# Kernel optimization log

Measured on AMD Instinct MI355X. Metric: run time of the kernel, lower is better.

## Reference

```python
import jax, jax.numpy as jnp
import numpy as np

S, B, R, H, TOP, CHL = 512, 32, 8, 128, 3, 19
I = CHL + 1  # GRU input size after null-channel concat


def setup_inputs() -> dict:
    key = jax.random.key(0)
    ks = jax.random.split(key, 12)
    f = lambda k, shp, sc=0.05: jax.random.normal(k, shp, dtype=jnp.float32) * sc
    return {
        "x": f(ks[0], (B, CHL, S), 1.0),
        "Wih": f(ks[1], (R, 3 * H, I)),      # per-rim GRU input weights (torch order r,z,n)
        "Whh": f(ks[2], (R, 3 * H, H)),      # per-rim GRU hidden weights
        "Qir_w": f(ks[3], (H, H)),
        "Qir_b": f(ks[4], (H,)),
        "Kir_w": f(ks[5], (H, S)),
        "Vir_w": f(ks[6], (H, S)),
        "Qrr_w": f(ks[7], (H, H)),
        "Krr_w": f(ks[8], (H, H)),
        "Vrr_w": f(ks[9], (H, H)),
    }


def reference(x, Wih, Whh, Qir_w, Qir_b, Kir_w, Vir_w, Qrr_w, Krr_w, Vrr_w):
    Bn = x.shape[0]
    # prepend null channel, reshape to (S, B, I)
    xc = jnp.concatenate([jnp.zeros((Bn, 1, x.shape[2]), x.dtype), x], axis=1)
    xs = jnp.transpose(xc, (2, 0, 1))  # (S, B, I)

    # ---- per-rim GRU (no bias), torch gate order (r, z, n) ----
    x_proj = jnp.einsum('sbi,rgi->srbg', xs, Wih)  # (S, R, B, 3H)

    def step(hprev, xp):
        hp = jnp.einsum('rbh,rgh->rbg', hprev, Whh)
        xr, xz, xn = jnp.split(xp, 3, axis=-1)
        hr, hz, hn = jnp.split(hp, 3, axis=-1)
        r = jax.nn.sigmoid(xr + hr)
        z = jax.nn.sigmoid(xz + hz)
        n = jnp.tanh(xn + r * hn)
        hnew = (1.0 - z) * n + z * hprev
        return hnew, hnew

    h0 = jnp.zeros((R, Bn, H), x.dtype)
    _, hs = jax.lax.scan(step, h0, x_proj)      # (S, R, B, H)
    h = jnp.transpose(hs, (1, 0, 2, 3))          # (R, S, B, H)

    # ---- stage one: input attention + rim competition ----
    x_bis = jnp.transpose(xs, (1, 2, 0))         # (B, I, S)
    q = jnp.einsum('rsbh,oh->rsbo', h, Qir_w) + Qir_b
    k = jnp.einsum('bis,os->bio', x_bis, Kir_w)
    v = jnp.einsum('bis,os->bio', x_bis, Vir_w)
    qk = jnp.einsum('rsbh,bih->sbri', q, k) / (H ** 0.5)
    soft = jax.nn.softmax(qk, axis=3)            # (S, B, R, I)
    idx = jax.lax.top_k(-soft[..., 0], TOP)[1]   # (S, B, TOP)
    mask = jnp.sum(jax.nn.one_hot(idx, R, dtype=jnp.float32), axis=-2)[..., None]  # (S,B,R,1)
    mask = jax.lax.stop_gradient(mask)
    qkv = jnp.einsum('sbri,bih->sbrh', soft, v)  # (S, B, R, H)

    # NoGrad: forward identity, backward grad*mask
    h1 = qkv * mask + jax.lax.stop_gradient(qkv * (1.0 - mask))

    # ---- stage two: rim-rim attention, masked ----
    q2 = jnp.einsum('sbrh,oh->sbro', h1, Qrr_w)
    k2 = jnp.einsum('sbrh,oh->sbro', h1, Krr_w)
    v2 = jnp.einsum('sbrh,oh->sbro', h1, Vrr_w)
    qk2 = jnp.einsum('sbrh,sbch->sbrc', q2, k2)  # (S, B, R, R), no scaling (as in source)
    soft2 = jax.nn.softmax(qk2, axis=3) * mask
    out = h1 + jnp.einsum('sbrc,sbch->sbrh', soft2, v2)
    return out * mask
```

## Files before the change

kernel.cpp:

```cpp
#include <hip/hip_runtime.h>
#include <math.h>


typedef float v2f __attribute__((ext_vector_type(2)));

#define PKF(acc, w, h) \
    asm("v_pk_fma_f32 %0, %1, %2, %0" : "+v"(acc) : "v"(w), "v"(h))

__global__ void kT(const float* __restrict__ Kir, const float* __restrict__ Vir,
                   const float* __restrict__ Vrr,
                   float* __restrict__ KirT, float* __restrict__ VirT,
                   float* __restrict__ VrrT) {
    int idx = blockIdx.x * 256 + threadIdx.x;
    if (idx < 65536) {
        int s = idx >> 7, o = idx & 127;
        KirT[idx] = Kir[o * 512 + s];
    } else if (idx < 131072) {
        int j = idx - 65536;
        int s = j >> 7, o = j & 127;
        VirT[j] = Vir[o * 512 + s];
    } else if (idx < 147456) {
        int j = idx - 131072;
        int g = j >> 7, h = j & 127;
        VrrT[j] = Vrr[h * 128 + g];
    }
}

__global__ __launch_bounds__(128) void kKV(const float* __restrict__ x,
        const float* __restrict__ KirT, const float* __restrict__ VirT,
        float* __restrict__ kbuf, float* __restrict__ vbuf) {
    const int b = blockIdx.x / 20, i = blockIdx.x % 20;
    const int o = threadIdx.x;
    if (i == 0) {
        kbuf[(b * 20) * 128 + o] = 0.0f;
        vbuf[(b * 20) * 128 + o] = 0.0f;
        return;
    }
    __shared__ float xL[512];
    for (int idx = threadIdx.x; idx < 512; idx += 128)
        xL[idx] = x[(b * 19 + (i - 1)) * 512 + idx];
    __syncthreads();
    float ak = 0.0f, av = 0.0f;
#pragma unroll 4
    for (int s = 0; s < 512; ++s) {
        float xv = xL[s];
        ak += xv * KirT[s * 128 + o];
        av += xv * VirT[s * 128 + o];
    }
    kbuf[(b * 20 + i) * 128 + o] = ak;
    vbuf[(b * 20 + i) * 128 + o] = av;
}

__global__ __launch_bounds__(128) void kKQ(const float* __restrict__ kbuf,
        const float* __restrict__ Qir, const float* __restrict__ Qib,
        float* __restrict__ KQ, float* __restrict__ cb) {
    const int b = blockIdx.x / 20, i = blockIdx.x % 20;
    const int h = threadIdx.x;
    __shared__ float kL[128];
    kL[h] = kbuf[(b * 20 + i) * 128 + h];
    __syncthreads();
    float acc = 0.0f;
#pragma unroll 4
    for (int o = 0; o < 128; ++o) acc += kL[o] * Qir[o * 128 + h];
    KQ[(b * 20 + i) * 128 + h] = acc;
    if (h == 0) {
        float c = 0.0f;
        for (int o = 0; o < 128; ++o) c += kL[o] * Qib[o];
        cb[b * 20 + i] = c;
    }
}

__global__ __launch_bounds__(256) void kM(const float* __restrict__ Qrr,
        const float* __restrict__ Krr, float* __restrict__ M) {
    const int h = blockIdx.x * 2 + (threadIdx.x >> 7);
    const int g = threadIdx.x & 127;
    float acc = 0.0f;
#pragma unroll 4
    for (int o = 0; o < 128; ++o) acc += Qrr[o * 128 + h] * Krr[o * 128 + g];
    M[h * 128 + g] = acc;
}

template<int CTRL>
__device__ __forceinline__ float dppadd(float v) {
    int r = __builtin_amdgcn_update_dpp(0, __float_as_int(v), CTRL, 0xF, 0xF, true);
    return v + __int_as_float(r);
}
template<int CTRL>
__device__ __forceinline__ float dppbcast(float v) {
    int r = __builtin_amdgcn_update_dpp(0, __float_as_int(v), CTRL, 0xF, 0xF, true);
    return __int_as_float(r);
}

__global__ __launch_bounds__(512, 2) void kGRU(const float* __restrict__ x,
        const float* __restrict__ Wih, const float* __restrict__ Whh,
        float* __restrict__ hs) {
    const int r = blockIdx.x >> 5;
    const int b = blockIdx.x & 31;
    const int t = threadIdx.x;
    const int j = t >> 2;
    const int kq = t & 3;

    __shared__ __align__(16) float xT[512 * 20];
    __shared__ __align__(16) float hsBuf[64 * 144];

    for (int idx = t; idx < 19 * 512; idx += 512) {
        int c = idx >> 9, s = idx & 511;
        xT[s * 20 + c] = x[(b * 19 + c) * 512 + s];
    }
    if (t < 144) hsBuf[63 * 144 + t] = 0.0f;

    v2f w0[16], w1[16], w2[16];
    {
        const float* Wb = Whh + (r * 384) * 128 + kq * 32;
        const v2f* s0p = (const v2f*)(Wb + (j) * 128);
        const v2f* s1p = (const v2f*)(Wb + (j + 128) * 128);
        const v2f* s2p = (const v2f*)(Wb + (j + 256) * 128);
#pragma unroll
        for (int u = 0; u < 16; ++u) {
            w0[u] = s0p[u];
            w1[u] = s1p[u];
            w2[u] = s2p[u];
        }
    }
    v2f wiv[9];
    float wlast;
    if (kq < 3) {
        const float* W = Wih + (r * 384 + (j + 128 * kq)) * 20;
#pragma unroll
        for (int c = 0; c < 9; ++c) wiv[c] = (v2f){W[2*c + 1], W[2*c + 2]};
        wlast = W[19];
    } else {
#pragma unroll
        for (int c = 0; c < 9; ++c) wiv[c] = (v2f){0.0f, 0.0f};
        wlast = 0.0f;
    }
    __syncthreads();

    const int jmap = j + ((j >> 5) << 2);
    const int cellBase = (b * 8 + r) * 128;
    float hprev = 0.0f;

    for (int s = 0; s < 512; ++s) {
        const int rowR = (s + 63) & 63;
        const v2f* hp2 = (const v2f*)(hsBuf + rowR * 144 + kq * 36);
        v2f hv[16];
#pragma unroll
        for (int u = 0; u < 16; ++u) hv[u] = hp2[u];

        float xp;
        {
            const v2f* xp2 = (const v2f*)(xT + s * 20);
            float x18 = xT[s * 20 + 18];
            v2f xacc = {0.0f, 0.0f};
            PKF(xacc, wiv[0], xp2[0]);
            PKF(xacc, wiv[1], xp2[1]);
            PKF(xacc, wiv[2], xp2[2]);
            PKF(xacc, wiv[3], xp2[3]);
            PKF(xacc, wiv[4], xp2[4]);
            PKF(xacc, wiv[5], xp2[5]);
            PKF(xacc, wiv[6], xp2[6]);
            PKF(xacc, wiv[7], xp2[7]);
            PKF(xacc, wiv[8], xp2[8]);
            xp = xacc[0] + xacc[1] + wlast * x18;
        }

        v2f a0 = {0.0f, 0.0f}, a1 = {0.0f, 0.0f}, a2 = {0.0f, 0.0f};
#pragma unroll
        for (int u = 0; u < 16; ++u) {
            v2f hh = hv[u];
            PKF(a0, w0[u], hh);
            PKF(a1, w1[u], hh);
            PKF(a2, w2[u], hh);
        }
        float p0 = a0[0] + a0[1];
        float p1 = a1[0] + a1[1];
        float p2 = a2[0] + a2[1];

        p0 = dppadd<0xB1>(p0); p1 = dppadd<0xB1>(p1); p2 = dppadd<0xB1>(p2);
        p0 = dppadd<0x4E>(p0); p1 = dppadd<0x4E>(p1); p2 = dppadd<0x4E>(p2);
        float xr = dppbcast<0x00>(xp);
        float xz = dppbcast<0x55>(xp);
        float xn = dppbcast<0xAA>(xp);

        float rg = __builtin_amdgcn_rcpf(1.0f + __expf(-(p0 + xr)));
        float zg = __builtin_amdgcn_rcpf(1.0f + __expf(-(p1 + xz)));
        float a  = xn + rg * p2;
        float ng = 1.0f - 2.0f * __builtin_amdgcn_rcpf(__expf(2.0f * a) + 1.0f);
        float hnew = ng + zg * (hprev - ng);
        hprev = hnew;
        if (kq == 0) hsBuf[(s & 63) * 144 + jmap] = hnew;
        __syncthreads();

        if ((s & 63) == 63) {
            const int sBase = s - 63;
            const int c4 = (t & 31) * 4;
            const int cm = c4 + ((c4 >> 5) << 2);
#pragma unroll
            for (int w = 0; w < 4; ++w) {
                int rr = (t >> 5) + w * 16;
                float4 v = *(const float4*)(hsBuf + rr * 144 + cm);
                *(float4*)(hs + (size_t)(sBase + rr) * 32768 + cellBase + c4) = v;
            }
            __syncthreads();
        }
    }
}

__global__ __launch_bounds__(256) void kS1(const float* __restrict__ hs,
        const float* __restrict__ KQ, const float* __restrict__ cb,
        const float* __restrict__ vbuf,
        float* __restrict__ h1, int* __restrict__ widx, float* __restrict__ out) {
    const int b = blockIdx.x & 31;
    const int s0 = (blockIdx.x >> 5) * 16;
    const int t = threadIdx.x;
    __shared__ float KQL[20 * 132];
    __shared__ float vL[20 * 128];
    __shared__ float cbL[20];
    __shared__ float hLt[8 * 132];
    __shared__ float qkL[8 * 20];
    __shared__ float sfL[8 * 20];
    __shared__ float s0L[8];
    __shared__ int wselL[3];

    for (int idx = t; idx < 2560; idx += 256) {
        int i = idx >> 7, h = idx & 127;
        KQL[i * 132 + h] = KQ[(b * 20 + i) * 128 + h];
        vL[i * 128 + h] = vbuf[(b * 20 + i) * 128 + h];
    }
    if (t < 20) cbL[t] = cb[b * 20 + t];
    __syncthreads();

    for (int p = 0; p < 16; ++p) {
        const int s = s0 + p;
        for (int idx = t; idx < 1024; idx += 256) {
            int r = idx >> 7, h = idx & 127;
            hLt[r * 132 + h] = hs[((s * 32 + b) * 8 + r) * 128 + h];
        }
        __syncthreads();
        if (t < 152) {
            int r = t / 19, i = t % 19 + 1;
            const float* hr = &hLt[r * 132];
            const float* kg = &KQL[i * 132];
            float a = 0.0f;
#pragma unroll 4
            for (int h = 0; h < 128; ++h) a += hr[h] * kg[h];
            qkL[r * 20 + i] = (a + cbL[i]) * 0.08838834764831845f;
        }
        if (t < 8) qkL[t * 20] = 0.0f;
        __syncthreads();
        if (t < 8) {
            float m = -3.4e38f;
            for (int i = 0; i < 20; ++i) m = fmaxf(m, qkL[t * 20 + i]);
            float sum = 0.0f;
            for (int i = 0; i < 20; ++i) {
                float e = expf(qkL[t * 20 + i] - m);
                sfL[t * 20 + i] = e;
                sum += e;
            }
            float inv = 1.0f / sum;
            for (int i = 0; i < 20; ++i) sfL[t * 20 + i] *= inv;
            s0L[t] = sfL[t * 20];
        }
        __syncthreads();
        if (t == 0) {
            unsigned chosen = 0;
            for (int n = 0; n < 3; ++n) {
                float best = 3.4e38f; int bi = 0;
                for (int r2 = 0; r2 < 8; ++r2) {
                    if (chosen & (1u << r2)) continue;
                    float v = s0L[r2];
                    if (v < best) { best = v; bi = r2; }
                }
                chosen |= (1u << bi);
                wselL[n] = bi;
                widx[(s * 32 + b) * 3 + n] = bi;
            }
        }
        __syncthreads();
        {
            const int h = t & 127, rq = t >> 7;
            float a0 = 0, a1 = 0, a2 = 0, a3 = 0;
            for (int i = 1; i < 20; ++i) {
                float vv = vL[i * 128 + h];
                a0 += sfL[(rq * 4 + 0) * 20 + i] * vv;
                a1 += sfL[(rq * 4 + 1) * 20 + i] * vv;
                a2 += sfL[(rq * 4 + 2) * 20 + i] * vv;
                a3 += sfL[(rq * 4 + 3) * 20 + i] * vv;
            }
            const int pairBase = (s * 32 + b) * 8;
            float av[4] = {a0, a1, a2, a3};
#pragma unroll
            for (int jj = 0; jj < 4; ++jj) {
                int rim = rq * 4 + jj;
                h1[(pairBase + rim) * 128 + h] = av[jj];
                bool win = (wselL[0] == rim) || (wselL[1] == rim) || (wselL[2] == rim);
                if (!win) out[(pairBase + rim) * 128 + h] = 0.0f;
            }
        }
        __syncthreads();
    }
}

template<int EPI>
__global__ __launch_bounds__(256) void kGemm(
        const float* __restrict__ Asrc,
        const float* __restrict__ Bm,
        const int* __restrict__ widx,
        const float* __restrict__ h1g,
        float* __restrict__ C) {
    __shared__ float ALt[64][132];
    __shared__ float BL[64][128];
    const int n0 = blockIdx.x * 128;
    const int t = threadIdx.x;
    const int tr = t >> 4, tc = t & 15;
    const int q0 = 2 * tc, q1 = 2 * tc + 1;
    const int bq0 = (q0 ^ (q0 >> 3)) * 4;
    const int bq1 = (q1 ^ (q1 >> 3)) * 4;
    float acc[8][8];
#pragma unroll
    for (int i = 0; i < 8; ++i)
#pragma unroll
        for (int jj = 0; jj < 8; ++jj) acc[i][jj] = 0.0f;

    for (int kc = 0; kc < 128; kc += 64) {
        __syncthreads();
#pragma unroll
        for (int i = 0; i < 8; ++i) {
            int idx = t + i * 256;
            int row = idx >> 4, qk = idx & 15;
            const float* src;
            if (EPI == 0) {
                int n = n0 + row;
                int pair = n / 3;
                int rim = widx[n];
                src = Asrc + ((pair << 3) + rim) * 128 + kc + qk * 4;
            } else {
                src = Asrc + (n0 + row) * 128 + kc + qk * 4;
            }
            float4 a = *(const float4*)src;
            ALt[qk * 4 + 0][row] = a.x;
            ALt[qk * 4 + 1][row] = a.y;
            ALt[qk * 4 + 2][row] = a.z;
            ALt[qk * 4 + 3][row] = a.w;
        }
#pragma unroll
        for (int i = 0; i < 8; ++i) {
            int idx = t + i * 256;
            int kk = idx >> 5, qc = idx & 31;
            float4 bv = *(const float4*)(Bm + (kc + kk) * 128 + qc * 4);
            int pos = (qc ^ (qc >> 3)) * 4;
            *(float4*)&BL[kk][pos] = bv;
        }
        __syncthreads();
#pragma unroll 2
        for (int k = 0; k < 64; ++k) {
            float4 a0 = *(const float4*)&ALt[k][8 * tr];
            float4 a1 = *(const float4*)&ALt[k][8 * tr + 4];
            float4 b0 = *(const float4*)&BL[k][bq0];
            float4 b1 = *(const float4*)&BL[k][bq1];
            float ar[8] = {a0.x, a0.y, a0.z, a0.w, a1.x, a1.y, a1.z, a1.w};
            float bc[8] = {b0.x, b0.y, b0.z, b0.w, b1.x, b1.y, b1.z, b1.w};
#pragma unroll
            for (int i = 0; i < 8; ++i)
#pragma unroll
                for (int jj = 0; jj < 8; ++jj) acc[i][jj] += ar[i] * bc[jj];
        }
    }
    if (EPI == 0) {
#pragma unroll
        for (int i = 0; i < 8; ++i) {
            int row = n0 + 8 * tr + i;
            *(float4*)(C + row * 128 + 8 * tc) =
                make_float4(acc[i][0], acc[i][1], acc[i][2], acc[i][3]);
            *(float4*)(C + row * 128 + 8 * tc + 4) =
                make_float4(acc[i][4], acc[i][5], acc[i][6], acc[i][7]);
        }
    } else {
#pragma unroll
        for (int i = 0; i < 8; ++i) {
            int n = n0 + 8 * tr + i;
            int pair = n / 3;
            int rim = widx[n];
            int base = ((pair << 3) + rim) * 128 + 8 * tc;
            float4 w0 = *(const float4*)(h1g + base);
            float4 w1 = *(const float4*)(h1g + base + 4);
            *(float4*)(C + base) = make_float4(acc[i][0] + w0.x, acc[i][1] + w0.y,
                                               acc[i][2] + w0.z, acc[i][3] + w0.w);
            *(float4*)(C + base + 4) = make_float4(acc[i][4] + w1.x, acc[i][5] + w1.y,
                                                   acc[i][6] + w1.z, acc[i][7] + w1.w);
        }
    }
}

__global__ __launch_bounds__(256) void kS2c(const float* __restrict__ T1,
        const float* __restrict__ h1, float* __restrict__ U) {
    const int w = threadIdx.x >> 6;
    const int lane = threadIdx.x & 63;
    const int p = blockIdx.x * 4 + w;
    const int base8 = p * 8 * 128;
    float hv0[8], hv1[8];
#pragma unroll
    for (int c = 0; c < 8; ++c) {
        hv0[c] = h1[base8 + c * 128 + lane];
        hv1[c] = h1[base8 + c * 128 + 64 + lane];
    }
    float t0[3], t1v[3];
#pragma unroll
    for (int wr = 0; wr < 3; ++wr) {
        t0[wr]  = T1[(p * 3 + wr) * 128 + lane];
        t1v[wr] = T1[(p * 3 + wr) * 128 + 64 + lane];
    }
    float pr[3][8];
#pragma unroll
    for (int wr = 0; wr < 3; ++wr)
#pragma unroll
        for (int c = 0; c < 8; ++c)
            pr[wr][c] = t0[wr] * hv0[c] + t1v[wr] * hv1[c];
#pragma unroll
    for (int off = 32; off > 0; off >>= 1)
#pragma unroll
        for (int wr = 0; wr < 3; ++wr)
#pragma unroll
            for (int c = 0; c < 8; ++c)
                pr[wr][c] += __shfl_xor(pr[wr][c], off, 64);
#pragma unroll
    for (int wr = 0; wr < 3; ++wr) {
        float m = pr[wr][0];
#pragma unroll
        for (int c = 1; c < 8; ++c) m = fmaxf(m, pr[wr][c]);
        float sum = 0.0f;
#pragma unroll
        for (int c = 0; c < 8; ++c) { pr[wr][c] = expf(pr[wr][c] - m); sum += pr[wr][c]; }
        float inv = 1.0f / sum;
        float u0 = 0.0f, u1 = 0.0f;
#pragma unroll
        for (int c = 0; c < 8; ++c) {
            float sv = pr[wr][c] * inv;
            u0 += sv * hv0[c];
            u1 += sv * hv1[c];
        }
        U[(p * 3 + wr) * 128 + lane] = u0;
        U[(p * 3 + wr) * 128 + 64 + lane] = u1;
    }
}

extern "C" void kernel_launch(void* const* d_in, const int* in_sizes, int n_in,
                              void* d_out, int out_size, void* d_ws, size_t ws_size,
                              hipStream_t stream) {
    const float* x   = (const float*)d_in[0];
    const float* Wih = (const float*)d_in[1];
    const float* Whh = (const float*)d_in[2];
    const float* Qir = (const float*)d_in[3];
    const float* Qib = (const float*)d_in[4];
    const float* Kir = (const float*)d_in[5];
    const float* Vir = (const float*)d_in[6];
    const float* Qrr = (const float*)d_in[7];
    const float* Krr = (const float*)d_in[8];
    const float* Vrr = (const float*)d_in[9];
    float* out = (float*)d_out;
    float* ws  = (float*)d_ws;

    float* hs   = ws;
    float* h1   = ws + 16777216;
    float* KirT = ws + 33554432;
    float* VirT = ws + 33619968;
    float* VrrT = ws + 33685504;
    float* kb   = ws + 33701888;
    float* vb   = ws + 33783808;
    float* KQ   = ws + 33865728;
    float* cb   = ws + 33947648;
    float* Mm   = ws + 33948288;
    int*   widx = (int*)(ws + 33964672);
    float* T1   = ws;
    float* U    = ws + 6291456;

    (void)in_sizes; (void)n_in; (void)out_size; (void)ws_size;

    kT  <<<576, 256, 0, stream>>>(Kir, Vir, Vrr, KirT, VirT, VrrT);
    kKV <<<640, 128, 0, stream>>>(x, KirT, VirT, kb, vb);
    kKQ <<<640, 128, 0, stream>>>(kb, Qir, Qib, KQ, cb);
    kM  <<<64, 256, 0, stream>>>(Qrr, Krr, Mm);
    kGRU<<<256, 512, 0, stream>>>(x, Wih, Whh, hs);
    kS1 <<<1024, 256, 0, stream>>>(hs, KQ, cb, vb, h1, widx, out);
    kGemm<0><<<384, 256, 0, stream>>>(h1, Mm, widx, nullptr, T1);
    kS2c<<<4096, 256, 0, stream>>>(T1, h1, U);
    kGemm<1><<<384, 256, 0, stream>>>(U, VrrT, widx, h1, out);
}
```

Baseline: 571.5 us.

## Stream GRU inputs from global memory per step and widen hidden-state LDS reads

Drops the shared-memory staging of the input sequence. Each step now reads the 19 input channels for the next timestep directly from global memory into registers, prefetched one step ahead, and computes the input projection with scalar FMAs. Hidden-state reads from LDS switch from 64-bit to 128-bit loads. This frees about 40KB of LDS and the upfront transpose loop, at the cost of strided uncached-pattern global loads on every step of the serial recurrence and more register pressure.

```diff
diff --git a/kernel.cpp b/kernel.cpp
--- a/kernel.cpp
+++ b/kernel.cpp
@@ -100,13 +100,8 @@
     const int j = t >> 2;
     const int kq = t & 3;
 
-    __shared__ __align__(16) float xT[512 * 20];
     __shared__ __align__(16) float hsBuf[64 * 144];
 
-    for (int idx = t; idx < 19 * 512; idx += 512) {
-        int c = idx >> 9, s = idx & 511;
-        xT[s * 20 + c] = x[(b * 19 + c) * 512 + s];
-    }
     if (t < 144) hsBuf[63 * 144 + t] = 0.0f;
 
     v2f w0[16], w1[16], w2[16];
@@ -122,17 +117,14 @@
             w2[u] = s2p[u];
         }
     }
-    v2f wiv[9];
-    float wlast;
+    float wi[19];
     if (kq < 3) {
         const float* W = Wih + (r * 384 + (j + 128 * kq)) * 20;
 #pragma unroll
-        for (int c = 0; c < 9; ++c) wiv[c] = (v2f){W[2*c + 1], W[2*c + 2]};
-        wlast = W[19];
+        for (int c = 0; c < 19; ++c) wi[c] = W[c + 1];
     } else {
 #pragma unroll
-        for (int c = 0; c < 9; ++c) wiv[c] = (v2f){0.0f, 0.0f};
-        wlast = 0.0f;
+        for (int c = 0; c < 19; ++c) wi[c] = 0.0f;
     }
     __syncthreads();
 
@@ -140,37 +132,39 @@
     const int cellBase = (b * 8 + r) * 128;
     float hprev = 0.0f;
 
+    const float* xb = x + b * 19 * 512;
+    float xs[19];
+#pragma unroll
+    for (int c = 0; c < 19; ++c) xs[c] = xb[c * 512];
+
     for (int s = 0; s < 512; ++s) {
         const int rowR = (s + 63) & 63;
-        const v2f* hp2 = (const v2f*)(hsBuf + rowR * 144 + kq * 36);
-        v2f hv[16];
-#pragma unroll
-        for (int u = 0; u < 16; ++u) hv[u] = hp2[u];
-
-        float xp;
-        {
-            const v2f* xp2 = (const v2f*)(xT + s * 20);
-            float x18 = xT[s * 20 + 18];
-            v2f xacc = {0.0f, 0.0f};
-            PKF(xacc, wiv[0], xp2[0]);
-            PKF(xacc, wiv[1], xp2[1]);
-            PKF(xacc, wiv[2], xp2[2]);
-            PKF(xacc, wiv[3], xp2[3]);
-            PKF(xacc, wiv[4], xp2[4]);
-            PKF(xacc, wiv[5], xp2[5]);
-            PKF(xacc, wiv[6], xp2[6]);
-            PKF(xacc, wiv[7], xp2[7]);
-            PKF(xacc, wiv[8], xp2[8]);
-            xp = xacc[0] + xacc[1] + wlast * x18;
+        const float4* hp4 = (const float4*)(hsBuf + rowR * 144 + kq * 36);
+        float4 hv4[8];
+#pragma unroll
+        for (int u = 0; u < 8; ++u) hv4[u] = hp4[u];
+
+        float xp = 0.0f;
+#pragma unroll
+        for (int c = 0; c < 19; ++c) xp += wi[c] * xs[c];
+
+        if (s < 511) {
+#pragma unroll
+            for (int c = 0; c < 19; ++c) xs[c] = xb[c * 512 + s + 1];
         }
 
         v2f a0 = {0.0f, 0.0f}, a1 = {0.0f, 0.0f}, a2 = {0.0f, 0.0f};
 #pragma unroll
-        for (int u = 0; u < 16; ++u) {
-            v2f hh = hv[u];
-            PKF(a0, w0[u], hh);
-            PKF(a1, w1[u], hh);
-            PKF(a2, w2[u], hh);
+        for (int u = 0; u < 8; ++u) {
+            float4 h4 = hv4[u];
+            v2f hl = (v2f){h4.x, h4.y};
+            v2f hh = (v2f){h4.z, h4.w};
+            PKF(a0, w0[2*u],   hl);
+            PKF(a1, w1[2*u],   hl);
+            PKF(a2, w2[2*u],   hl);
+            PKF(a0, w0[2*u+1], hh);
+            PKF(a1, w1[2*u+1], hh);
+            PKF(a2, w2[2*u+1], hh);
         }
         float p0 = a0[0] + a0[1];
         float p1 = a1[0] + a1[1];
```

Result: slower. 611.7 us (+7.0%).
